# Optimization experiments

Measured on AMD Instinct MI355X. Metric: run time of the kernel, lower is better.

Reference implementation:

```python
import jax, jax.numpy as jnp
import numpy as np

B, L, C = 2, 2048, 1024
H = 16
D = C // H  # 64
MAX_SCALE_MUL = float(np.log(100.0))
EPS = 1e-12


def setup_inputs() -> dict:
    key = jax.random.key(0)
    ks = jax.random.split(key, 6)
    x = jax.random.normal(ks[0], (B, L, C), dtype=jnp.float32)
    attn_bias = jax.random.normal(ks[1], (1, 1, L, L), dtype=jnp.float32) * 0.02
    W_qkv = jax.random.normal(ks[2], (3 * C, C), dtype=jnp.float32) * (1.0 / np.sqrt(C))
    q_bias = jnp.zeros((C,), dtype=jnp.float32)
    v_bias = jnp.zeros((C,), dtype=jnp.float32)
    scale_mul = jnp.full((1, H, 1, 1), np.log(4.0), dtype=jnp.float32)
    W_proj = jax.random.normal(ks[3], (C, C), dtype=jnp.float32) * (1.0 / np.sqrt(C))
    b_proj = jnp.zeros((C,), dtype=jnp.float32)
    return {"x": x, "attn_bias": attn_bias, "W_qkv": W_qkv, "q_bias": q_bias,
            "v_bias": v_bias, "scale_mul": scale_mul, "W_proj": W_proj, "b_proj": b_proj}


def _l2norm(t):
    # F.normalize(dim=-1): x / max(||x||_2, eps)
    n = jnp.sqrt(jnp.sum(t * t, axis=-1, keepdims=True))
    return t / jnp.maximum(n, EPS)


def reference(x, attn_bias, W_qkv, q_bias, v_bias, scale_mul, W_proj, b_proj):
    bias = jnp.concatenate([q_bias, jnp.zeros_like(q_bias), v_bias])  # (3C,)
    qkv = x @ W_qkv.T + bias                     # (B, L, 3C)
    qkv = qkv.reshape(B, L, 3, H, D)
    q, k, v = jnp.moveaxis(qkv, 2, 0)            # each (B, L, H, D)
    q = jnp.transpose(q, (0, 2, 1, 3))           # (B, H, L, D)
    k = jnp.transpose(k, (0, 2, 1, 3))
    v = jnp.transpose(v, (0, 2, 1, 3))
    # attn_l2_norm path: scale = 1, learned per-head scale clamped at log(100)
    sm = jnp.exp(jnp.minimum(scale_mul, MAX_SCALE_MUL))  # (1, H, 1, 1)
    q = _l2norm(q) * sm
    k = _l2norm(k)
    scores = jnp.einsum('bhqd,bhkd->bhqk', q, k) + attn_bias  # scale=1
    attn = jax.nn.softmax(scores, axis=-1)
    out = jnp.einsum('bhqk,bhkd->bhqd', attn, v)  # (B, H, L, D)
    out = jnp.transpose(out, (0, 2, 1, 3)).reshape(B, L, C)
    return out @ W_proj.T + b_proj
```

## Files before the change

### kernel.cpp

```cpp
#include <hip/hip_runtime.h>


typedef __bf16 bf16x8 __attribute__((ext_vector_type(8)));
typedef __bf16 bf16x4 __attribute__((ext_vector_type(4)));
typedef float  f32x4  __attribute__((ext_vector_type(4)));

#define BB 2
#define LL 2048
#define CC 1024
#define HH 16
#define DD 64
#define LOG2E 1.44269504088896f

__device__ __forceinline__ f32x4 mfma_16x16x32(bf16x8 a, bf16x8 b, f32x4 c) {
    return __builtin_amdgcn_mfma_f32_16x16x32_bf16(a, b, c, 0, 0, 0);
}

__global__ __launch_bounds__(256) void cvt_bf16_kernel(const float* __restrict__ in,
                                                       __bf16* __restrict__ out, int n4) {
    int i = blockIdx.x * 256 + threadIdx.x;
    if (i >= n4) return;
    float4 v = reinterpret_cast<const float4*>(in)[i];
    bf16x4 o;
    o[0] = (__bf16)v.x; o[1] = (__bf16)v.y; o[2] = (__bf16)v.z; o[3] = (__bf16)v.w;
    reinterpret_cast<bf16x4*>(out)[i] = o;
}

__global__ __launch_bounds__(256) void bias_prep_kernel(const float* __restrict__ bias,
                                                        __bf16* __restrict__ bias_bf) {
    __shared__ float wmax[4];
    const int l = blockIdx.x, tid = threadIdx.x;
    const int w = tid >> 6;
    float4 a = reinterpret_cast<const float4*>(bias + (size_t)l * 2048)[tid];
    float4 b = reinterpret_cast<const float4*>(bias + (size_t)l * 2048 + 1024)[tid];
    float m = fmaxf(fmaxf(fmaxf(a.x, a.y), fmaxf(a.z, a.w)),
                    fmaxf(fmaxf(b.x, b.y), fmaxf(b.z, b.w)));
#pragma unroll
    for (int off = 1; off < 64; off <<= 1) m = fmaxf(m, __shfl_xor(m, off, 64));
    if ((tid & 63) == 0) wmax[w] = m;
    __syncthreads();
    float M = fmaxf(fmaxf(wmax[0], wmax[1]), fmaxf(wmax[2], wmax[3]));
    bf16x4 o0, o1;
    o0[0] = (__bf16)(a.x - M); o0[1] = (__bf16)(a.y - M);
    o0[2] = (__bf16)(a.z - M); o0[3] = (__bf16)(a.w - M);
    o1[0] = (__bf16)(b.x - M); o1[1] = (__bf16)(b.y - M);
    o1[2] = (__bf16)(b.z - M); o1[3] = (__bf16)(b.w - M);
    reinterpret_cast<bf16x4*>(bias_bf + (size_t)l * 2048)[tid] = o0;
    reinterpret_cast<bf16x4*>(bias_bf + (size_t)l * 2048 + 1024)[tid] = o1;
}

template <int OUT_MODE>
__global__ __launch_bounds__(256) void gemm_bt_kernel(
    const __bf16* __restrict__ A, const __bf16* __restrict__ Bm,
    float* __restrict__ Cf, __bf16* __restrict__ Cb,
    const float* __restrict__ bias, int M, int N, int K) {
    __shared__ __bf16 As[128 * 64];
    __shared__ __bf16 Bs[128 * 64];
    const int tid = threadIdx.x;
    const int m0 = blockIdx.x * 128, n0 = blockIdx.y * 128;
    const int w  = tid >> 6, l = tid & 63;
    const int wr = (w >> 1) * 64, wc = (w & 1) * 64;
    const int lr = l & 15, lg = l >> 4;
    const int rmask = (lr & 7) << 4;
    f32x4 acc[4][4] = {};
    const int srow = tid >> 1;
    const int scb  = (tid & 1) * 64;
    const int smask = (srow & 7) << 4;
    const __bf16* ag = A  + (size_t)(m0 + srow) * K + (tid & 1) * 32;
    const __bf16* bg = Bm + (size_t)(n0 + srow) * K + (tid & 1) * 32;
    char* asb = (char*)As + srow * 128;
    char* bsb = (char*)Bs + srow * 128;

    for (int kt = 0; kt < K; kt += 64) {
        bf16x8 av[4], bv[4];
#pragma unroll
        for (int j = 0; j < 4; ++j) {
            av[j] = *reinterpret_cast<const bf16x8*>(ag + kt + j * 8);
            bv[j] = *reinterpret_cast<const bf16x8*>(bg + kt + j * 8);
        }
        __syncthreads();
#pragma unroll
        for (int j = 0; j < 4; ++j) {
            *reinterpret_cast<bf16x8*>(asb + ((scb + j * 16) ^ smask)) = av[j];
            *reinterpret_cast<bf16x8*>(bsb + ((scb + j * 16) ^ smask)) = bv[j];
        }
        __syncthreads();
#pragma unroll
        for (int kk = 0; kk < 2; ++kk) {
            bf16x8 af[4], bfr[4];
#pragma unroll
            for (int m = 0; m < 4; ++m)
                af[m] = *reinterpret_cast<const bf16x8*>(
                    (char*)As + (wr + m * 16 + lr) * 128 + ((kk * 64 + lg * 16) ^ rmask));
#pragma unroll
            for (int n = 0; n < 4; ++n)
                bfr[n] = *reinterpret_cast<const bf16x8*>(
                    (char*)Bs + (wc + n * 16 + lr) * 128 + ((kk * 64 + lg * 16) ^ rmask));
#pragma unroll
            for (int m = 0; m < 4; ++m)
#pragma unroll
                for (int n = 0; n < 4; ++n)
                    acc[m][n] = mfma_16x16x32(af[m], bfr[n], acc[m][n]);
        }
    }
#pragma unroll
    for (int m = 0; m < 4; ++m) {
#pragma unroll
        for (int n = 0; n < 4; ++n) {
            const int row = m0 + wr + m * 16 + lg * 4;
            const int col = n0 + wc + n * 16 + lr;
#pragma unroll
            for (int r = 0; r < 4; ++r) {
                float v = acc[m][n][r];
                if (OUT_MODE == 0) {
                    Cb[(size_t)(row + r) * N + col] = (__bf16)v;
                } else {
                    Cf[(size_t)(row + r) * N + col] = v + bias[col];
                }
            }
        }
    }
}

__global__ __launch_bounds__(256) void qkv_norm_kernel(
    const __bf16* __restrict__ qkv, const float* __restrict__ q_bias,
    const float* __restrict__ v_bias, const float* __restrict__ scale_mul,
    __bf16* __restrict__ Q, __bf16* __restrict__ K, __bf16* __restrict__ V) {
    const int bl = blockIdx.x;
    const int tid = threadIdx.x;
    const int w = tid >> 6, d = tid & 63;
    const int b = bl >> 11, l = bl & 2047;
    for (int g = w; g < 48; g += 4) {
        const int s = g >> 4, h = g & 15;
        float v = (float)qkv[(size_t)bl * 3072 + g * 64 + d];
        if (s == 0) v += q_bias[h * 64 + d];
        if (s == 2) v += v_bias[h * 64 + d];
        if (s < 2) {
            float ss = v * v;
#pragma unroll
            for (int off = 1; off < 64; off <<= 1) ss += __shfl_xor(ss, off, 64);
            float nrm = sqrtf(ss);
            v = v / fmaxf(nrm, 1e-12f);
            if (s == 0) v *= __expf(fminf(scale_mul[h], 4.60517019f));
        }
        __bf16* dst = (s == 0) ? Q : ((s == 1) ? K : V);
        dst[((size_t)(b * 16 + h) * 2048 + l) * 64 + d] = (__bf16)v;
    }
}

__global__ __launch_bounds__(256) void v_transpose_kernel(const __bf16* __restrict__ Vin,
                                                          __bf16* __restrict__ Vt) {
    __shared__ __bf16 T[64][72];
    const int lb = blockIdx.x, bh = blockIdx.y;
    const int tid = threadIdx.x;
    const size_t base = (size_t)bh * LL * DD;
    const int row = tid >> 2, c = (tid & 3) * 16;
    {
        const __bf16* src = Vin + base + (size_t)(lb * 64 + row) * 64 + c;
        *reinterpret_cast<bf16x8*>(&T[row][c])     = *reinterpret_cast<const bf16x8*>(src);
        *reinterpret_cast<bf16x8*>(&T[row][c + 8]) = *reinterpret_cast<const bf16x8*>(src + 8);
    }
    __syncthreads();
    bf16x8 o0, o1;
#pragma unroll
    for (int j = 0; j < 8; ++j) {
        o0[j] = T[c + j][row];
        o1[j] = T[c + 8 + j][row];
    }
    __bf16* dst = Vt + base + (size_t)row * 2048 + lb * 64 + c;
    *reinterpret_cast<bf16x8*>(dst)     = o0;
    *reinterpret_cast<bf16x8*>(dst + 8) = o1;
}

__global__ __launch_bounds__(256) void attn_kernel(
    const __bf16* __restrict__ Q, const __bf16* __restrict__ K,
    const __bf16* __restrict__ Vt, const __bf16* __restrict__ bias_bf,
    const float* __restrict__ scale_mul, __bf16* __restrict__ Octx) {
    __shared__ __bf16 KVs[2][2][64 * 64];
    __shared__ __bf16 Ps[64 * 64];
    const int bh = blockIdx.x, qb = blockIdx.y;
    const int tid = threadIdx.x;
    const int w = tid >> 6, l = tid & 63;
    const int lr = l & 15, lg = l >> 4;
    const int rmask = (lr & 7) << 4;
    const int b = bh >> 4, h = bh & 15;
    const size_t base = (size_t)bh * LL * DD;
    const float smh = __expf(fminf(scale_mul[h], 4.60517019f));
    const float cexp = -smh * LOG2E;

    const int gq = qb * 64 + w * 16 + lr;
    bf16x8 qf[2];
    qf[0] = *reinterpret_cast<const bf16x8*>(Q + base + (size_t)gq * 64 + lg * 8);
    qf[1] = *reinterpret_cast<const bf16x8*>(Q + base + (size_t)gq * 64 + 32 + lg * 8);
    const __bf16* brow = bias_bf + (size_t)gq * 2048;

    const int srow = tid >> 2;
    const int scb  = (tid & 3) * 32;
    const int smask = (srow & 7) << 4;
    const __bf16* kgbase = K  + base + (size_t)srow * 64   + (tid & 3) * 16;
    const __bf16* vgbase = Vt + base + (size_t)srow * 2048 + (tid & 3) * 16;

    bf16x8 k0, k1, v0, v1;
    auto stage_regs = [&](int kb) {
        const __bf16* kg = kgbase + (size_t)kb * 64 * 64;
        k0 = *reinterpret_cast<const bf16x8*>(kg);
        k1 = *reinterpret_cast<const bf16x8*>(kg + 8);
        const __bf16* vg = vgbase + kb * 64;
        v0 = *reinterpret_cast<const bf16x8*>(vg);
        v1 = *reinterpret_cast<const bf16x8*>(vg + 8);
    };
    auto write_lds = [&](int buf) {
        char* kp = (char*)KVs[buf][0] + srow * 128;
        char* vp = (char*)KVs[buf][1] + srow * 128;
        *reinterpret_cast<bf16x8*>(kp + (scb ^ smask))        = k0;
        *reinterpret_cast<bf16x8*>(kp + ((scb + 16) ^ smask)) = k1;
        *reinterpret_cast<bf16x8*>(vp + (scb ^ smask))        = v0;
        *reinterpret_cast<bf16x8*>(vp + ((scb + 16) ^ smask)) = v1;
    };

    stage_regs(0);
    write_lds(0);

    f32x4 Oa[4] = {};
    float lsum = 0.f;
    int cur = 0;
    char* psb = (char*)Ps + (w * 16 + lr) * 128;

    for (int kb = 0; kb < 32; ++kb) {
        __syncthreads();
        if (kb < 31) stage_regs(kb + 1);

        const char* Kc = (const char*)KVs[cur][0];
        const char* Vc = (const char*)KVs[cur][1];

        f32x4 sa[4] = {};
#pragma unroll
        for (int t = 0; t < 4; ++t) {
            const char* kr = Kc + (t * 16 + lr) * 128;
            bf16x8 kf0 = *reinterpret_cast<const bf16x8*>(kr + ((lg * 16) ^ rmask));
            bf16x8 kf1 = *reinterpret_cast<const bf16x8*>(kr + ((64 + lg * 16) ^ rmask));
            sa[t] = mfma_16x16x32(kf0, qf[0], sa[t]);
            sa[t] = mfma_16x16x32(kf1, qf[1], sa[t]);
        }

#pragma unroll
        for (int t = 0; t < 4; ++t) {
            bf16x4 bv = *reinterpret_cast<const bf16x4*>(brow + kb * 64 + t * 16 + lg * 4);
            bf16x4 pb;
#pragma unroll
            for (int r = 0; r < 4; ++r) {
                float s = sa[t][r] + (float)bv[r];
                float p = exp2f(fmaf(s, LOG2E, cexp));
                lsum += p;
                pb[r] = (__bf16)p;
            }
            *reinterpret_cast<bf16x4*>(psb + ((t * 32 + lg * 8) ^ rmask)) = pb;
        }

        bf16x8 pf0 = *reinterpret_cast<const bf16x8*>(psb + ((lg * 16) ^ rmask));
        bf16x8 pf1 = *reinterpret_cast<const bf16x8*>(psb + ((64 + lg * 16) ^ rmask));
#pragma unroll
        for (int t = 0; t < 4; ++t) {
            const char* vr = Vc + (t * 16 + lr) * 128;
            bf16x8 vf0 = *reinterpret_cast<const bf16x8*>(vr + ((lg * 16) ^ rmask));
            bf16x8 vf1 = *reinterpret_cast<const bf16x8*>(vr + ((64 + lg * 16) ^ rmask));
            Oa[t] = mfma_16x16x32(pf0, vf0, Oa[t]);
            Oa[t] = mfma_16x16x32(pf1, vf1, Oa[t]);
        }

        if (kb < 31) write_lds(cur ^ 1);
        cur ^= 1;
    }

    lsum += __shfl_xor(lsum, 16, 64);
    lsum += __shfl_xor(lsum, 32, 64);
    float inv[4];
#pragma unroll
    for (int r = 0; r < 4; ++r) inv[r] = 1.0f / __shfl(lsum, lg * 4 + r, 64);

#pragma unroll
    for (int t = 0; t < 4; ++t)
#pragma unroll
        for (int r = 0; r < 4; ++r) {
            const int row = qb * 64 + w * 16 + lg * 4 + r;
            float o = Oa[t][r] * inv[r];
            Octx[((size_t)(b * 2048 + row)) * 1024 + h * 64 + t * 16 + lr] = (__bf16)o;
        }
}

extern "C" void kernel_launch(void* const* d_in, const int* in_sizes, int n_in,
                              void* d_out, int out_size, void* d_ws, size_t ws_size,
                              hipStream_t stream) {
    const float* x         = (const float*)d_in[0];
    const float* attn_bias = (const float*)d_in[1];
    const float* W_qkv     = (const float*)d_in[2];
    const float* q_bias    = (const float*)d_in[3];
    const float* v_bias    = (const float*)d_in[4];
    const float* scale_mul = (const float*)d_in[5];
    const float* W_proj    = (const float*)d_in[6];
    const float* b_proj    = (const float*)d_in[7];
    float* out = (float*)d_out;

    char* ws = (char*)d_ws;
    size_t off = 0;
    auto alloc = [&](size_t bytes) {
        void* p = ws + off;
        off = (off + bytes + 255) & ~(size_t)255;
        return p;
    };
    __bf16* xb     = (__bf16*)alloc((size_t)4096 * 1024 * 2);
    __bf16* wqkvb  = (__bf16*)alloc((size_t)3072 * 1024 * 2);
    __bf16* wprojb = (__bf16*)alloc((size_t)1024 * 1024 * 2);
    __bf16* qkvb   = (__bf16*)alloc((size_t)4096 * 3072 * 2);
    __bf16* Qw     = (__bf16*)alloc((size_t)BB * HH * LL * DD * 2);
    __bf16* Kw     = (__bf16*)alloc((size_t)BB * HH * LL * DD * 2);
    __bf16* Vw     = (__bf16*)alloc((size_t)BB * HH * LL * DD * 2);
    __bf16* Oc     = (__bf16*)alloc((size_t)4096 * 1024 * 2);
    __bf16* bias_bf = qkvb;
    __bf16* Vt      = qkvb + (size_t)2048 * 2048;

    cvt_bf16_kernel<<<4096, 256, 0, stream>>>(x, xb, 4096 * 1024 / 4);
    cvt_bf16_kernel<<<3072, 256, 0, stream>>>(W_qkv, wqkvb, 3072 * 1024 / 4);
    cvt_bf16_kernel<<<1024, 256, 0, stream>>>(W_proj, wprojb, 1024 * 1024 / 4);

    gemm_bt_kernel<0><<<dim3(32, 24), 256, 0, stream>>>(
        xb, wqkvb, nullptr, qkvb, nullptr, 4096, 3072, 1024);

    qkv_norm_kernel<<<4096, 256, 0, stream>>>(qkvb, q_bias, v_bias, scale_mul, Qw, Kw, Vw);

    bias_prep_kernel<<<2048, 256, 0, stream>>>(attn_bias, bias_bf);
    v_transpose_kernel<<<dim3(32, 32), 256, 0, stream>>>(Vw, Vt);

    attn_kernel<<<dim3(32, 32), 256, 0, stream>>>(Qw, Kw, Vt, bias_bf, scale_mul, Oc);

    gemm_bt_kernel<1><<<dim3(32, 8), 256, 0, stream>>>(
        Oc, wprojb, out, nullptr, b_proj, 4096, 1024, 1024);
}
```

Measured before the change: 196.9 us.

## Double query rows per attention block, prescale by log2e, async GEMM LDS loads

The attention kernel now handles 128 query rows per block, so each wave processes two 16-row groups that share every K/V tile read from LDS, and the grid is halved. Log2e is folded into Q and the prepared bias, and the bias plus offset is used as the MFMA accumulator seed, which removes the per-element FMA before exp2. The GEMM switches to direct global-to-LDS loads with an XOR swizzle, dropping the register staging but waiting on vmcnt(0) with no prefetch overlap. The attention launch bound asks for 3 blocks per CU, which can constrain registers now that accumulators are doubled, and the halved grid gives fewer blocks to fill the GPU.

```diff
diff --git a/kernel.cpp b/kernel.cpp
--- a/kernel.cpp
+++ b/kernel.cpp
@@ -14,6 +14,13 @@
 
 __device__ __forceinline__ f32x4 mfma_16x16x32(bf16x8 a, bf16x8 b, f32x4 c) {
     return __builtin_amdgcn_mfma_f32_16x16x32_bf16(a, b, c, 0, 0, 0);
+}
+
+__device__ __forceinline__ void gload_lds16(const __bf16* g, __bf16* lds) {
+    __builtin_amdgcn_global_load_lds(
+        (const __attribute__((address_space(1))) unsigned int*)g,
+        (__attribute__((address_space(3))) unsigned int*)lds,
+        16, 0, 0);
 }
 
 __global__ __launch_bounds__(256) void cvt_bf16_kernel(const float* __restrict__ in,
@@ -41,10 +48,10 @@
     __syncthreads();
     float M = fmaxf(fmaxf(wmax[0], wmax[1]), fmaxf(wmax[2], wmax[3]));
     bf16x4 o0, o1;
-    o0[0] = (__bf16)(a.x - M); o0[1] = (__bf16)(a.y - M);
-    o0[2] = (__bf16)(a.z - M); o0[3] = (__bf16)(a.w - M);
-    o1[0] = (__bf16)(b.x - M); o1[1] = (__bf16)(b.y - M);
-    o1[2] = (__bf16)(b.z - M); o1[3] = (__bf16)(b.w - M);
+    o0[0] = (__bf16)((a.x - M) * LOG2E); o0[1] = (__bf16)((a.y - M) * LOG2E);
+    o0[2] = (__bf16)((a.z - M) * LOG2E); o0[3] = (__bf16)((a.w - M) * LOG2E);
+    o1[0] = (__bf16)((b.x - M) * LOG2E); o1[1] = (__bf16)((b.y - M) * LOG2E);
+    o1[2] = (__bf16)((b.z - M) * LOG2E); o1[3] = (__bf16)((b.w - M) * LOG2E);
     reinterpret_cast<bf16x4*>(bias_bf + (size_t)l * 2048)[tid] = o0;
     reinterpret_cast<bf16x4*>(bias_bf + (size_t)l * 2048 + 1024)[tid] = o1;
 }
@@ -63,27 +70,18 @@
     const int lr = l & 15, lg = l >> 4;
     const int rmask = (lr & 7) << 4;
     f32x4 acc[4][4] = {};
-    const int srow = tid >> 1;
-    const int scb  = (tid & 1) * 64;
-    const int smask = (srow & 7) << 4;
-    const __bf16* ag = A  + (size_t)(m0 + srow) * K + (tid & 1) * 32;
-    const __bf16* bg = Bm + (size_t)(n0 + srow) * K + (tid & 1) * 32;
-    char* asb = (char*)As + srow * 128;
-    char* bsb = (char*)Bs + srow * 128;
+    const int lrow = l >> 3;
+    const int celem = (((l & 7) ^ lrow) << 3);
 
     for (int kt = 0; kt < K; kt += 64) {
-        bf16x8 av[4], bv[4];
-#pragma unroll
-        for (int j = 0; j < 4; ++j) {
-            av[j] = *reinterpret_cast<const bf16x8*>(ag + kt + j * 8);
-            bv[j] = *reinterpret_cast<const bf16x8*>(bg + kt + j * 8);
-        }
         __syncthreads();
 #pragma unroll
-        for (int j = 0; j < 4; ++j) {
-            *reinterpret_cast<bf16x8*>(asb + ((scb + j * 16) ^ smask)) = av[j];
-            *reinterpret_cast<bf16x8*>(bsb + ((scb + j * 16) ^ smask)) = bv[j];
-        }
+        for (int i = 0; i < 4; ++i) {
+            const int row = w * 32 + i * 8;
+            gload_lds16(A + (size_t)(m0 + row + lrow) * K + kt + celem, &As[row * 64]);
+            gload_lds16(Bm + (size_t)(n0 + row + lrow) * K + kt + celem, &Bs[row * 64]);
+        }
+        asm volatile("s_waitcnt vmcnt(0)" ::: "memory");
         __syncthreads();
 #pragma unroll
         for (int kk = 0; kk < 2; ++kk) {
@@ -141,7 +139,7 @@
             for (int off = 1; off < 64; off <<= 1) ss += __shfl_xor(ss, off, 64);
             float nrm = sqrtf(ss);
             v = v / fmaxf(nrm, 1e-12f);
-            if (s == 0) v *= __expf(fminf(scale_mul[h], 4.60517019f));
+            if (s == 0) v *= __expf(fminf(scale_mul[h], 4.60517019f)) * LOG2E;
         }
         __bf16* dst = (s == 0) ? Q : ((s == 1) ? K : V);
         dst[((size_t)(b * 16 + h) * 2048 + l) * 64 + d] = (__bf16)v;
@@ -172,9 +170,9 @@
     *reinterpret_cast<bf16x8*>(dst + 8) = o1;
 }
 
-__global__ __launch_bounds__(256) void attn_kernel(
+__global__ __launch_bounds__(256, 3) void attn_kernel(
     const __bf16* __restrict__ Q, const __bf16* __restrict__ K,
-    const __bf16* __restrict__ Vt, const __bf16* __restrict__ bias_bf,
+    const __bf16* __restrict__ Vt, const __bf16* __restrict__ biasL,
     const float* __restrict__ scale_mul, __bf16* __restrict__ Octx) {
     __shared__ __bf16 KVs[2][2][64 * 64];
     __shared__ __bf16 Ps[64 * 64];
@@ -188,11 +186,14 @@
     const float smh = __expf(fminf(scale_mul[h], 4.60517019f));
     const float cexp = -smh * LOG2E;
 
-    const int gq = qb * 64 + w * 16 + lr;
-    bf16x8 qf[2];
-    qf[0] = *reinterpret_cast<const bf16x8*>(Q + base + (size_t)gq * 64 + lg * 8);
-    qf[1] = *reinterpret_cast<const bf16x8*>(Q + base + (size_t)gq * 64 + 32 + lg * 8);
-    const __bf16* brow = bias_bf + (size_t)gq * 2048;
+    const int gq0 = qb * 128 + w * 32 + lr;
+    bf16x8 qf0[2], qf1[2];
+    qf0[0] = *reinterpret_cast<const bf16x8*>(Q + base + (size_t)gq0 * 64 + lg * 8);
+    qf0[1] = *reinterpret_cast<const bf16x8*>(Q + base + (size_t)gq0 * 64 + 32 + lg * 8);
+    qf1[0] = *reinterpret_cast<const bf16x8*>(Q + base + (size_t)(gq0 + 16) * 64 + lg * 8);
+    qf1[1] = *reinterpret_cast<const bf16x8*>(Q + base + (size_t)(gq0 + 16) * 64 + 32 + lg * 8);
+    const __bf16* brow0 = biasL + (size_t)gq0 * 2048 + lg * 4;
+    const __bf16* brow1 = biasL + (size_t)(gq0 + 16) * 2048 + lg * 4;
 
     const int srow = tid >> 2;
     const int scb  = (tid & 3) * 32;
@@ -221,8 +222,8 @@
     stage_regs(0);
     write_lds(0);
 
-    f32x4 Oa[4] = {};
-    float lsum = 0.f;
+    f32x4 Oa0[4] = {}, Oa1[4] = {};
+    float ls0 = 0.f, ls1 = 0.f;
     int cur = 0;
     char* psb = (char*)Ps + (w * 16 + lr) * 128;
 
@@ -230,61 +231,106 @@
         __syncthreads();
         if (kb < 31) stage_regs(kb + 1);
 
+        bf16x4 b0[4], b1[4];
+#pragma unroll
+        for (int t = 0; t < 4; ++t) {
+            b0[t] = *reinterpret_cast<const bf16x4*>(brow0 + kb * 64 + t * 16);
+            b1[t] = *reinterpret_cast<const bf16x4*>(brow1 + kb * 64 + t * 16);
+        }
+
         const char* Kc = (const char*)KVs[cur][0];
         const char* Vc = (const char*)KVs[cur][1];
 
-        f32x4 sa[4] = {};
+        f32x4 sa0[4], sa1[4];
+#pragma unroll
+        for (int t = 0; t < 4; ++t)
+#pragma unroll
+            for (int r = 0; r < 4; ++r) {
+                sa0[t][r] = (float)b0[t][r] + cexp;
+                sa1[t][r] = (float)b1[t][r] + cexp;
+            }
+
 #pragma unroll
         for (int t = 0; t < 4; ++t) {
             const char* kr = Kc + (t * 16 + lr) * 128;
             bf16x8 kf0 = *reinterpret_cast<const bf16x8*>(kr + ((lg * 16) ^ rmask));
             bf16x8 kf1 = *reinterpret_cast<const bf16x8*>(kr + ((64 + lg * 16) ^ rmask));
-            sa[t] = mfma_16x16x32(kf0, qf[0], sa[t]);
-            sa[t] = mfma_16x16x32(kf1, qf[1], sa[t]);
+            sa0[t] = mfma_16x16x32(kf0, qf0[0], sa0[t]);
+            sa0[t] = mfma_16x16x32(kf1, qf0[1], sa0[t]);
+            sa1[t] = mfma_16x16x32(kf0, qf1[0], sa1[t]);
+            sa1[t] = mfma_16x16x32(kf1, qf1[1], sa1[t]);
         }
 
 #pragma unroll
         for (int t = 0; t < 4; ++t) {
-            bf16x4 bv = *reinterpret_cast<const bf16x4*>(brow + kb * 64 + t * 16 + lg * 4);
             bf16x4 pb;
 #pragma unroll
             for (int r = 0; r < 4; ++r) {
-                float s = sa[t][r] + (float)bv[r];
-                float p = exp2f(fmaf(s, LOG2E, cexp));
-                lsum += p;
+                float p = exp2f(sa0[t][r]);
+                ls0 += p;
                 pb[r] = (__bf16)p;
             }
             *reinterpret_cast<bf16x4*>(psb + ((t * 32 + lg * 8) ^ rmask)) = pb;
         }
-
-        bf16x8 pf0 = *reinterpret_cast<const bf16x8*>(psb + ((lg * 16) ^ rmask));
-        bf16x8 pf1 = *reinterpret_cast<const bf16x8*>(psb + ((64 + lg * 16) ^ rmask));
+        {
+            bf16x8 pf0 = *reinterpret_cast<const bf16x8*>(psb + ((lg * 16) ^ rmask));
+            bf16x8 pf1 = *reinterpret_cast<const bf16x8*>(psb + ((64 + lg * 16) ^ rmask));
+#pragma unroll
+            for (int t = 0; t < 4; ++t) {
+                const char* vr = Vc + (t * 16 + lr) * 128;
+                bf16x8 vf0 = *reinterpret_cast<const bf16x8*>(vr + ((lg * 16) ^ rmask));
+                bf16x8 vf1 = *reinterpret_cast<const bf16x8*>(vr + ((64 + lg * 16) ^ rmask));
+                Oa0[t] = mfma_16x16x32(pf0, vf0, Oa0[t]);
+                Oa0[t] = mfma_16x16x32(pf1, vf1, Oa0[t]);
+            }
+        }
+
 #pragma unroll
         for (int t = 0; t < 4; ++t) {
-            const char* vr = Vc + (t * 16 + lr) * 128;
-            bf16x8 vf0 = *reinterpret_cast<const bf16x8*>(vr + ((lg * 16) ^ rmask));
-            bf16x8 vf1 = *reinterpret_cast<const bf16x8*>(vr + ((64 + lg * 16) ^ rmask));
-            Oa[t] = mfma_16x16x32(pf0, vf0, Oa[t]);
-            Oa[t] = mfma_16x16x32(pf1, vf1, Oa[t]);
+            bf16x4 pb;
+#pragma unroll
+            for (int r = 0; r < 4; ++r) {
+                float p = exp2f(sa1[t][r]);
+                ls1 += p;
+                pb[r] = (__bf16)p;
+            }
+            *reinterpret_cast<bf16x4*>(psb + ((t * 32 + lg * 8) ^ rmask)) = pb;
+        }
+        {
+            bf16x8 pf0 = *reinterpret_cast<const bf16x8*>(psb + ((lg * 16) ^ rmask));
+            bf16x8 pf1 = *reinterpret_cast<const bf16x8*>(psb + ((64 + lg * 16) ^ rmask));
+#pragma unroll
+            for (int t = 0; t < 4; ++t) {
+                const char* vr = Vc + (t * 16 + lr) * 128;
+                bf16x8 vf0 = *reinterpret_cast<const bf16x8*>(vr + ((lg * 16) ^ rmask));
+                bf16x8 vf1 = *reinterpret_cast<const bf16x8*>(vr + ((64 + lg * 16) ^ rmask));
+                Oa1[t] = mfma_16x16x32(pf0, vf0, Oa1[t]);
+                Oa1[t] = mfma_16x16x32(pf1, vf1, Oa1[t]);
+            }
         }
 
         if (kb < 31) write_lds(cur ^ 1);
         cur ^= 1;
     }
 
-    lsum += __shfl_xor(lsum, 16, 64);
-    lsum += __shfl_xor(lsum, 32, 64);
-    float inv[4];
-#pragma unroll
-    for (int r = 0; r < 4; ++r) inv[r] = 1.0f / __shfl(lsum, lg * 4 + r, 64);
+    ls0 += __shfl_xor(ls0, 16, 64); ls0 += __shfl_xor(ls0, 32, 64);
+    ls1 += __shfl_xor(ls1, 16, 64); ls1 += __shfl_xor(ls1, 32, 64);
+    float inv0[4], inv1[4];
+#pragma unroll
+    for (int r = 0; r < 4; ++r) {
+        inv0[r] = 1.0f / __shfl(ls0, lg * 4 + r, 64);
+        inv1[r] = 1.0f / __shfl(ls1, lg * 4 + r, 64);
+    }
 
 #pragma unroll
     for (int t = 0; t < 4; ++t)
 #pragma unroll
         for (int r = 0; r < 4; ++r) {
-            const int row = qb * 64 + w * 16 + lg * 4 + r;
-            float o = Oa[t][r] * inv[r];
-            Octx[((size_t)(b * 2048 + row)) * 1024 + h * 64 + t * 16 + lr] = (__bf16)o;
+            const int row0 = qb * 128 + w * 32 + lg * 4 + r;
+            Octx[((size_t)(b * 2048 + row0)) * 1024 + h * 64 + t * 16 + lr] =
+                (__bf16)(Oa0[t][r] * inv0[r]);
+            Octx[((size_t)(b * 2048 + row0 + 16)) * 1024 + h * 64 + t * 16 + lr] =
+                (__bf16)(Oa1[t][r] * inv1[r]);
         }
 }
 
@@ -331,7 +377,7 @@
     bias_prep_kernel<<<2048, 256, 0, stream>>>(attn_bias, bias_bf);
     v_transpose_kernel<<<dim3(32, 32), 256, 0, stream>>>(Vw, Vt);
 
-    attn_kernel<<<dim3(32, 32), 256, 0, stream>>>(Qw, Kw, Vt, bias_bf, scale_mul, Oc);
+    attn_kernel<<<dim3(32, 16), 256, 0, stream>>>(Qw, Kw, Vt, bias_bf, scale_mul, Oc);
 
     gemm_bt_kernel<1><<<dim3(32, 8), 256, 0, stream>>>(
         Oc, wprojb, out, nullptr, b_proj, 4096, 1024, 1024);
```

After: 209.3 us. +6.3%, slower.

## Keep softmax P in registers, prefetch bias, async LDS loads and swizzled GEMM grid

Applied to the files above, without the earlier changes.

The attention kernel now feeds the exp'd scores straight from registers into the PV MFMA. It permutes the V fragment reads to match, which removes the P round-trip through shared memory. The bias is pre-scaled by log2e and prefetched one tile ahead, and log2e is folded into Q so that bias plus the constant seed the accumulator. The GEMM switches to direct global-to-LDS loads with a swizzled layout and remaps workgroups for L2 locality. Attention gets a launch bound of 4 blocks per CU. This adds register pressure, and the async loads are not overlapped with compute because of the full vmcnt wait.

```diff
diff --git a/kernel.cpp b/kernel.cpp
--- a/kernel.cpp
+++ b/kernel.cpp
@@ -14,6 +14,19 @@
 
 __device__ __forceinline__ f32x4 mfma_16x16x32(bf16x8 a, bf16x8 b, f32x4 c) {
     return __builtin_amdgcn_mfma_f32_16x16x32_bf16(a, b, c, 0, 0, 0);
+}
+
+__device__ __forceinline__ void gload_lds16(const __bf16* g, __bf16* lds) {
+    __builtin_amdgcn_global_load_lds(
+        (const __attribute__((address_space(1))) unsigned int*)g,
+        (__attribute__((address_space(3))) unsigned int*)lds,
+        16, 0, 0);
+}
+
+__device__ __forceinline__ unsigned pk_bf16(float a, float b) {
+    unsigned short ua = __builtin_bit_cast(unsigned short, (__bf16)a);
+    unsigned short ub = __builtin_bit_cast(unsigned short, (__bf16)b);
+    return (unsigned)ua | ((unsigned)ub << 16);
 }
 
 __global__ __launch_bounds__(256) void cvt_bf16_kernel(const float* __restrict__ in,
@@ -41,10 +54,10 @@
     __syncthreads();
     float M = fmaxf(fmaxf(wmax[0], wmax[1]), fmaxf(wmax[2], wmax[3]));
     bf16x4 o0, o1;
-    o0[0] = (__bf16)(a.x - M); o0[1] = (__bf16)(a.y - M);
-    o0[2] = (__bf16)(a.z - M); o0[3] = (__bf16)(a.w - M);
-    o1[0] = (__bf16)(b.x - M); o1[1] = (__bf16)(b.y - M);
-    o1[2] = (__bf16)(b.z - M); o1[3] = (__bf16)(b.w - M);
+    o0[0] = (__bf16)((a.x - M) * LOG2E); o0[1] = (__bf16)((a.y - M) * LOG2E);
+    o0[2] = (__bf16)((a.z - M) * LOG2E); o0[3] = (__bf16)((a.w - M) * LOG2E);
+    o1[0] = (__bf16)((b.x - M) * LOG2E); o1[1] = (__bf16)((b.y - M) * LOG2E);
+    o1[2] = (__bf16)((b.z - M) * LOG2E); o1[3] = (__bf16)((b.w - M) * LOG2E);
     reinterpret_cast<bf16x4*>(bias_bf + (size_t)l * 2048)[tid] = o0;
     reinterpret_cast<bf16x4*>(bias_bf + (size_t)l * 2048 + 1024)[tid] = o1;
 }
@@ -57,33 +70,27 @@
     __shared__ __bf16 As[128 * 64];
     __shared__ __bf16 Bs[128 * 64];
     const int tid = threadIdx.x;
-    const int m0 = blockIdx.x * 128, n0 = blockIdx.y * 128;
+    const int nwg = gridDim.x * gridDim.y;
+    const int flat = blockIdx.y * gridDim.x + blockIdx.x;
+    const int wg = (flat & 7) * (nwg >> 3) + (flat >> 3);
+    const int m0 = (wg % gridDim.x) * 128, n0 = (wg / gridDim.x) * 128;
     const int w  = tid >> 6, l = tid & 63;
     const int wr = (w >> 1) * 64, wc = (w & 1) * 64;
     const int lr = l & 15, lg = l >> 4;
     const int rmask = (lr & 7) << 4;
     f32x4 acc[4][4] = {};
-    const int srow = tid >> 1;
-    const int scb  = (tid & 1) * 64;
-    const int smask = (srow & 7) << 4;
-    const __bf16* ag = A  + (size_t)(m0 + srow) * K + (tid & 1) * 32;
-    const __bf16* bg = Bm + (size_t)(n0 + srow) * K + (tid & 1) * 32;
-    char* asb = (char*)As + srow * 128;
-    char* bsb = (char*)Bs + srow * 128;
+    const int lrow = l >> 3;
+    const int celem = (((l & 7) ^ lrow) << 3);
 
     for (int kt = 0; kt < K; kt += 64) {
-        bf16x8 av[4], bv[4];
-#pragma unroll
-        for (int j = 0; j < 4; ++j) {
-            av[j] = *reinterpret_cast<const bf16x8*>(ag + kt + j * 8);
-            bv[j] = *reinterpret_cast<const bf16x8*>(bg + kt + j * 8);
-        }
         __syncthreads();
 #pragma unroll
-        for (int j = 0; j < 4; ++j) {
-            *reinterpret_cast<bf16x8*>(asb + ((scb + j * 16) ^ smask)) = av[j];
-            *reinterpret_cast<bf16x8*>(bsb + ((scb + j * 16) ^ smask)) = bv[j];
-        }
+        for (int i = 0; i < 4; ++i) {
+            const int row = w * 32 + i * 8;
+            gload_lds16(A + (size_t)(m0 + row + lrow) * K + kt + celem, &As[row * 64]);
+            gload_lds16(Bm + (size_t)(n0 + row + lrow) * K + kt + celem, &Bs[row * 64]);
+        }
+        asm volatile("s_waitcnt vmcnt(0)" ::: "memory");
         __syncthreads();
 #pragma unroll
         for (int kk = 0; kk < 2; ++kk) {
@@ -141,7 +148,7 @@
             for (int off = 1; off < 64; off <<= 1) ss += __shfl_xor(ss, off, 64);
             float nrm = sqrtf(ss);
             v = v / fmaxf(nrm, 1e-12f);
-            if (s == 0) v *= __expf(fminf(scale_mul[h], 4.60517019f));
+            if (s == 0) v *= __expf(fminf(scale_mul[h], 4.60517019f)) * LOG2E;
         }
         __bf16* dst = (s == 0) ? Q : ((s == 1) ? K : V);
         dst[((size_t)(b * 16 + h) * 2048 + l) * 64 + d] = (__bf16)v;
@@ -172,12 +179,11 @@
     *reinterpret_cast<bf16x8*>(dst + 8) = o1;
 }
 
-__global__ __launch_bounds__(256) void attn_kernel(
+__global__ __launch_bounds__(256, 4) void attn_kernel(
     const __bf16* __restrict__ Q, const __bf16* __restrict__ K,
-    const __bf16* __restrict__ Vt, const __bf16* __restrict__ bias_bf,
+    const __bf16* __restrict__ Vt, const __bf16* __restrict__ biasL,
     const float* __restrict__ scale_mul, __bf16* __restrict__ Octx) {
     __shared__ __bf16 KVs[2][2][64 * 64];
-    __shared__ __bf16 Ps[64 * 64];
     const int bh = blockIdx.x, qb = blockIdx.y;
     const int tid = threadIdx.x;
     const int w = tid >> 6, l = tid & 63;
@@ -192,7 +198,7 @@
     bf16x8 qf[2];
     qf[0] = *reinterpret_cast<const bf16x8*>(Q + base + (size_t)gq * 64 + lg * 8);
     qf[1] = *reinterpret_cast<const bf16x8*>(Q + base + (size_t)gq * 64 + 32 + lg * 8);
-    const __bf16* brow = bias_bf + (size_t)gq * 2048;
+    const __bf16* brow = biasL + (size_t)gq * 2048 + lg * 4;
 
     const int srow = tid >> 2;
     const int scb  = (tid & 3) * 32;
@@ -224,16 +230,33 @@
     f32x4 Oa[4] = {};
     float lsum = 0.f;
     int cur = 0;
-    char* psb = (char*)Ps + (w * 16 + lr) * 128;
+
+    bf16x4 bcur[4];
+#pragma unroll
+    for (int t = 0; t < 4; ++t)
+        bcur[t] = *reinterpret_cast<const bf16x4*>(brow + t * 16);
 
     for (int kb = 0; kb < 32; ++kb) {
         __syncthreads();
         if (kb < 31) stage_regs(kb + 1);
 
+        bf16x4 bnext[4];
+        if (kb < 31) {
+#pragma unroll
+            for (int t = 0; t < 4; ++t)
+                bnext[t] = *reinterpret_cast<const bf16x4*>(brow + (kb + 1) * 64 + t * 16);
+        }
+
         const char* Kc = (const char*)KVs[cur][0];
         const char* Vc = (const char*)KVs[cur][1];
 
-        f32x4 sa[4] = {};
+        f32x4 sa[4];
+#pragma unroll
+        for (int t = 0; t < 4; ++t)
+#pragma unroll
+            for (int r = 0; r < 4; ++r)
+                sa[t][r] = (float)bcur[t][r] + cexp;
+
 #pragma unroll
         for (int t = 0; t < 4; ++t) {
             const char* kr = Kc + (t * 16 + lr) * 128;
@@ -243,32 +266,37 @@
             sa[t] = mfma_16x16x32(kf1, qf[1], sa[t]);
         }
 
-#pragma unroll
-        for (int t = 0; t < 4; ++t) {
-            bf16x4 bv = *reinterpret_cast<const bf16x4*>(brow + kb * 64 + t * 16 + lg * 4);
-            bf16x4 pb;
+        float p[4][4];
+#pragma unroll
+        for (int t = 0; t < 4; ++t)
 #pragma unroll
             for (int r = 0; r < 4; ++r) {
-                float s = sa[t][r] + (float)bv[r];
-                float p = exp2f(fmaf(s, LOG2E, cexp));
-                lsum += p;
-                pb[r] = (__bf16)p;
+                p[t][r] = exp2f(sa[t][r]);
+                lsum += p[t][r];
             }
-            *reinterpret_cast<bf16x4*>(psb + ((t * 32 + lg * 8) ^ rmask)) = pb;
-        }
-
-        bf16x8 pf0 = *reinterpret_cast<const bf16x8*>(psb + ((lg * 16) ^ rmask));
-        bf16x8 pf1 = *reinterpret_cast<const bf16x8*>(psb + ((64 + lg * 16) ^ rmask));
+        union Upa { unsigned u[4]; bf16x8 v; } pa0, pa1;
+        pa0.u[0] = pk_bf16(p[0][0], p[0][1]); pa0.u[1] = pk_bf16(p[0][2], p[0][3]);
+        pa0.u[2] = pk_bf16(p[1][0], p[1][1]); pa0.u[3] = pk_bf16(p[1][2], p[1][3]);
+        pa1.u[0] = pk_bf16(p[2][0], p[2][1]); pa1.u[1] = pk_bf16(p[2][2], p[2][3]);
+        pa1.u[2] = pk_bf16(p[3][0], p[3][1]); pa1.u[3] = pk_bf16(p[3][2], p[3][3]);
+
 #pragma unroll
         for (int t = 0; t < 4; ++t) {
             const char* vr = Vc + (t * 16 + lr) * 128;
-            bf16x8 vf0 = *reinterpret_cast<const bf16x8*>(vr + ((lg * 16) ^ rmask));
-            bf16x8 vf1 = *reinterpret_cast<const bf16x8*>(vr + ((64 + lg * 16) ^ rmask));
-            Oa[t] = mfma_16x16x32(pf0, vf0, Oa[t]);
-            Oa[t] = mfma_16x16x32(pf1, vf1, Oa[t]);
-        }
-
-        if (kb < 31) write_lds(cur ^ 1);
+            union Uv { uint2 d[2]; bf16x8 v; } vf0, vf1;
+            vf0.d[0] = *reinterpret_cast<const uint2*>(vr + ((lg * 8) ^ rmask));
+            vf0.d[1] = *reinterpret_cast<const uint2*>(vr + ((32 + lg * 8) ^ rmask));
+            vf1.d[0] = *reinterpret_cast<const uint2*>(vr + ((64 + lg * 8) ^ rmask));
+            vf1.d[1] = *reinterpret_cast<const uint2*>(vr + ((96 + lg * 8) ^ rmask));
+            Oa[t] = mfma_16x16x32(pa0.v, vf0.v, Oa[t]);
+            Oa[t] = mfma_16x16x32(pa1.v, vf1.v, Oa[t]);
+        }
+
+        if (kb < 31) {
+            write_lds(cur ^ 1);
+#pragma unroll
+            for (int t = 0; t < 4; ++t) bcur[t] = bnext[t];
+        }
         cur ^= 1;
     }
 
```

After: 197.7 us. Within noise of the previous version (+0.4%).
